# Kernel tuning notes

Measured on AMD Instinct MI355X. Metric: run time of the kernel, lower is better.

## Reference

```python
import jax, jax.numpy as jnp
import numpy as np

WIDTH = 1.0  # radial_width
AMPLITUDE = (WIDTH ** 0.5) * 1.772637204826652  # ~sqrt(pi*width)
BN_EPS = 1e-3  # keras BatchNormalization default


def sine_pos_encoding(seq_len, hidden, dtype):
    # keras_nlp.layers.SinePositionEncoding, max_wavelength=10000
    position = jnp.arange(seq_len, dtype=dtype)
    min_freq = jnp.asarray(1.0 / 10000.0, dtype)
    timescales = min_freq ** (2 * (jnp.arange(hidden) // 2).astype(dtype) / hidden)
    angles = position[:, None] * timescales[None, :]  # [T, H]
    odd = (jnp.arange(hidden) % 2).astype(dtype)
    return jnp.sin(angles) * (1 - odd) + jnp.cos(angles) * odd


def setup_inputs() -> dict:
    key = jax.random.key(0)
    ks = jax.random.split(key, 4)
    B, T, C, F, K, L = 16, 4096, 8, 64, 11, 4096
    x = jax.random.normal(ks[0], (B, T, C), jnp.float32)
    conv_w = jax.random.normal(ks[1], (K, C, F), jnp.float32) * 0.1
    conv_b = jnp.zeros((F,), jnp.float32)
    gamma = jnp.ones((F,), jnp.float32)
    beta = jnp.zeros((F,), jnp.float32)
    mean = jnp.zeros((F,), jnp.float32)
    var = jnp.ones((F,), jnp.float32)
    # HeNormal init for dense
    dense_w = jax.random.normal(ks[2], (F, L), jnp.float32) * (2.0 / F) ** 0.5
    dense_b = jnp.zeros((L,), jnp.float32)
    return dict(x=x, conv_w=conv_w, conv_b=conv_b, gamma=gamma, beta=beta,
                mean=mean, var=var, dense_w=dense_w, dense_b=dense_b)


def reference(x, conv_w, conv_b, gamma, beta, mean, var, dense_w, dense_b):
    B, T, C = x.shape
    F = conv_w.shape[-1]
    L = dense_w.shape[-1]
    # Conv1D same padding -> [B, T, F]
    h = jax.lax.conv_general_dilated(x, conv_w, (1,), 'SAME',
                                     dimension_numbers=('NWC', 'WIO', 'NWC')) + conv_b
    # BatchNorm (inference form)
    h = (h - mean) / jnp.sqrt(var + BN_EPS) * gamma + beta
    # Softmax over time axis
    h = jax.nn.softmax(h, axis=1)
    # sine positional encoding added
    h = h + sine_pos_encoding(T, F, x.dtype)
    # Dense with sigmoid, rescale to [-1, 1]
    d = jax.nn.sigmoid(h @ dense_w + dense_b) * 2.0 - 1.0  # [B, T, L]
    # ReductionLayer: sum over time -> shift weights [B, L]
    shift = jnp.sum(d, axis=1)
    # ShiftingLayer: Gaussian RBF warp matrix then matmul
    idx_in = jnp.arange(1, T + 1, dtype=x.dtype)                       # [T]
    scale = jnp.asarray(T / L, x.dtype)
    idx_sh = (jnp.arange(1, L + 1, dtype=x.dtype) + shift) * scale     # [B, L]
    M = idx_in[None, None, :] - idx_sh[:, :, None]                     # [B, L, T]
    M = jnp.exp(-(M * M) / WIDTH) / AMPLITUDE
    return jnp.matmul(M, x)  # [B, L, C]
```

## Files before the change

### kernel.cpp

```cpp
#include <hip/hip_runtime.h>
#include <stdint.h>

#define BB 16
#define TT 4096
#define CC 8
#define FF 64
#define KW 11
#define LL 4096

#define L2E 1.442695040888963f
#define NCONV (BB * (TT / 64))

typedef __attribute__((ext_vector_type(8))) short short8;
typedef __attribute__((ext_vector_type(16))) float floatx16;

__device__ float e_buf[(size_t)BB * TT * FF];
__device__ float sumpart[NCONV * FF];
__device__ float shift_part[(size_t)BB * 32 * LL];

__device__ __forceinline__ unsigned short f2b(float f) {
    union { float f; uint32_t i; } v; v.f = f;
    uint32_t x = v.i;
    return (unsigned short)((x + 0x7fffu + ((x >> 16) & 1u)) >> 16);
}
__device__ __forceinline__ float b2f(unsigned short u) {
    union { uint32_t i; float f; } v; v.i = ((uint32_t)u) << 16; return v.f;
}

#define DOT8(acc, ra, rb, wp) \
    acc = fmaf(ra.x, (wp)[0], acc); acc = fmaf(ra.y, (wp)[1], acc); \
    acc = fmaf(ra.z, (wp)[2], acc); acc = fmaf(ra.w, (wp)[3], acc); \
    acc = fmaf(rb.x, (wp)[4], acc); acc = fmaf(rb.y, (wp)[5], acc); \
    acc = fmaf(rb.z, (wp)[6], acc); acc = fmaf(rb.w, (wp)[7], acc);

__global__ __launch_bounds__(256) void k_convsplit(
        const float* __restrict__ x, const float* __restrict__ cw,
        const float* __restrict__ cb, const float* __restrict__ gm,
        const float* __restrict__ bt, const float* __restrict__ mn,
        const float* __restrict__ vr, const float* __restrict__ dw,
        unsigned short* __restrict__ Wt) {
    if (blockIdx.x >= NCONV) {
        const int idx  = (blockIdx.x - NCONV) * 256 + threadIdx.x;
        const int j    = idx & 7;
        const int ln   = (idx >> 3) & 31;
        const int half = (idx >> 8) & 1;
        const int kf   = (idx >> 9) & 3;
        const int lt   = idx >> 11;
        const int l = lt * 32 + ln;
        const int k = kf * 16 + half * 8 + j;
        const float v = dw[(size_t)k * LL + l] * (-L2E);
        const unsigned short hi = f2b(v);
        const unsigned short lo = f2b(v - b2f(hi));
        Wt[idx] = hi;
        Wt[262144 + idx] = lo;
        return;
    }
    __shared__ __align__(16) float xsm[(64 + KW - 1) * CC];
    __shared__ float red[4 * FF];
    const int tid = threadIdx.x;
    const int b  = blockIdx.x / (TT / 64);
    const int t0 = (blockIdx.x % (TT / 64)) * 64;
    const int f = tid & 63, ts = tid >> 6;

    float wreg[KW * CC];
#pragma unroll
    for (int kc = 0; kc < KW * CC; ++kc) wreg[kc] = cw[kc * FF + f];

    for (int i = tid; i < (64 + KW - 1) * CC; i += 256) {
        int row = i >> 3, c = i & 7;
        int t = t0 - (KW / 2) + row;
        xsm[i] = (t >= 0 && t < TT) ? x[((size_t)b * TT + t) * CC + c] : 0.0f;
    }
    const float s  = gm[f] * rsqrtf(vr[f] + 1e-3f);
    const float bb = bt[f] + (cb[f] - mn[f]) * s;
    const float s2 = s * L2E, b2 = bb * L2E;
    __syncthreads();

    float* eb = e_buf + ((size_t)b * TT + t0) * FF + f;
    const float4* xv = (const float4*)xsm;
    float esum = 0.f;
#pragma unroll 1
    for (int c = 0; c < 4; ++c) {
        const int tb = c * 16 + ts * 4;
        float a0 = 0.f, a1 = 0.f, a2 = 0.f, a3 = 0.f;
#pragma unroll
        for (int k = 0; k < KW + 3; ++k) {
            const float4 ra = xv[(tb + k) * 2];
            const float4 rb = xv[(tb + k) * 2 + 1];
            if (k <= 10)           { DOT8(a0, ra, rb, wreg + k * 8); }
            if (k >= 1 && k <= 11) { DOT8(a1, ra, rb, wreg + (k - 1) * 8); }
            if (k >= 2 && k <= 12) { DOT8(a2, ra, rb, wreg + (k - 2) * 8); }
            if (k >= 3)            { DOT8(a3, ra, rb, wreg + (k - 3) * 8); }
        }
        float e0 = __builtin_amdgcn_exp2f(fmaf(a0, s2, b2));
        float e1 = __builtin_amdgcn_exp2f(fmaf(a1, s2, b2));
        float e2 = __builtin_amdgcn_exp2f(fmaf(a2, s2, b2));
        float e3 = __builtin_amdgcn_exp2f(fmaf(a3, s2, b2));
        eb[(tb + 0) * FF] = e0;
        eb[(tb + 1) * FF] = e1;
        eb[(tb + 2) * FF] = e2;
        eb[(tb + 3) * FF] = e3;
        esum += (e0 + e1) + (e2 + e3);
    }
    red[ts * FF + f] = esum;
    __syncthreads();
    if (ts == 0)
        sumpart[blockIdx.x * FF + f] = red[f] + red[FF + f] + red[2 * FF + f] + red[3 * FF + f];
}

__global__ __launch_bounds__(512) void k_main(
        const unsigned short* __restrict__ Wt,
        const float* __restrict__ db, float* __restrict__ dummy) {
    __shared__ __align__(16) unsigned short As[16384];

    const int tid = threadIdx.x;
    const int b  = blockIdx.y;
    const int t0 = blockIdx.x * 128;
    const int f = tid & 63, tq = tid >> 6;

    float se = 0.f;
    const float* sp = sumpart + (size_t)b * 64 * FF + f;
#pragma unroll 8
    for (int j = 0; j < 64; ++j) se += sp[j * FF];
    const float inv_se = 1.0f / se;

    const float tsf = exp2f(-0.20762050586796017f * (float)(f & ~1));
    const int kfh = ((f >> 4) << 1) | ((f >> 3) & 1);
    const int jj  = f & 7;
    const float ang0 = (float)(t0 + tq) * tsf;
    const float dA = 8.0f * tsf;
    float sv = sinf(ang0), cv = cosf(ang0);
    const float sd = sinf(dA), cd = cosf(dA);

    const float* eb = e_buf + ((size_t)b * TT + t0) * FF + f;
#pragma unroll 4
    for (int i = 0; i < 16; ++i) {
        const int tt = tq + 8 * i;
        float ev = eb[tt * FF];
        float p = (f & 1) ? cv : sv;
        float h = fmaf(ev, inv_se, p);
        const unsigned short hi = f2b(h);
        const unsigned short lo = f2b(h - b2f(hi));
        const int off = ((tt >> 5) * 8 + kfh) * 256 + (tt & 31) * 8 + jj;
        As[off] = hi;
        As[8192 + off] = lo;
        float ns = fmaf(sv, cd, cv * sd);
        float nc = fmaf(cv, cd, -(sv * sd));
        sv = ns; cv = nc;
    }
    __syncthreads();

    const int lane = tid & 63;
    const int wv   = tid >> 6;
    const int half = lane >> 5;
    const int ln31 = lane & 31;
    const int vbase = (half << 9) | (ln31 << 4);
    const char* Ab = (const char*)As;
    const char* Wb = (const char*)Wt;

#pragma unroll 1
    for (int i = 0; i < 16; ++i) {
        const int lt = (i + 2 * wv) & 15;
        const int ltile = lt * 8 + wv;
        const int lbase = ltile * 32;
        const char* wp = Wb + ((size_t)ltile << 12) + vbase;
        short8 Whi[4], Wlo[4];
#pragma unroll
        for (int kf = 0; kf < 4; ++kf) {
            Whi[kf] = *reinterpret_cast<const short8*>(wp + kf * 1024);
            Wlo[kf] = *reinterpret_cast<const short8*>(wp + 524288 + kf * 1024);
        }
        const float dbn = db[lbase + ln31] * (-L2E);

        float ss[4] = {0.f, 0.f, 0.f, 0.f};
#pragma unroll
        for (int nt = 0; nt < 4; ++nt) {
            floatx16 acc;
#pragma unroll
            for (int r = 0; r < 16; ++r) acc[r] = dbn;
            __builtin_amdgcn_s_setprio(1);
#pragma unroll
            for (int kf = 0; kf < 4; ++kf) {
                const int ao = (nt * 8 + kf * 2) << 9;
                short8 Ahi = *reinterpret_cast<const short8*>(Ab + ao + vbase);
                short8 Alo = *reinterpret_cast<const short8*>(Ab + 16384 + ao + vbase);
                acc = __builtin_amdgcn_mfma_f32_32x32x16_bf16(Ahi, Whi[kf], acc, 0, 0, 0);
                acc = __builtin_amdgcn_mfma_f32_32x32x16_bf16(Alo, Whi[kf], acc, 0, 0, 0);
                acc = __builtin_amdgcn_mfma_f32_32x32x16_bf16(Ahi, Wlo[kf], acc, 0, 0, 0);
            }
            __builtin_amdgcn_s_setprio(0);
#pragma unroll
            for (int q = 0; q < 4; ++q) {
                float e0 = __builtin_amdgcn_exp2f(acc[4 * q + 0]);
                float e1 = __builtin_amdgcn_exp2f(acc[4 * q + 1]);
                float e2 = __builtin_amdgcn_exp2f(acc[4 * q + 2]);
                float e3 = __builtin_amdgcn_exp2f(acc[4 * q + 3]);
                float a0 = 1.f + e0, a1 = 1.f + e1, a2 = 1.f + e2, a3 = 1.f + e3;
                float p01 = a0 * a1, p23 = a2 * a3;
                float num = fmaf(a0 + a1, p23, (a2 + a3) * p01);
                ss[q] = fmaf(num, __builtin_amdgcn_rcpf(p01 * p23), ss[q]);
            }
        }
        float ssum = (ss[0] + ss[1]) + (ss[2] + ss[3]);
        ssum += __shfl_xor(ssum, 32);
        if (half == 0)
            shift_part[((size_t)b * 32 + blockIdx.x) * LL + lbase + ln31] = ssum;
    }
}

__global__ __launch_bounds__(256) void k_warp(
        const float* __restrict__ x, float* __restrict__ out) {
    const int idx = blockIdx.x * 256 + threadIdx.x;
    const int l = idx & (LL - 1);
    const int b = idx >> 12;
    float S = 0.f;
    const float* sp = shift_part + (size_t)b * 32 * LL + l;
#pragma unroll 8
    for (int tt = 0; tt < 32; ++tt) S += sp[tt * LL];
    const float sh = fmaf(2.0f, S, -(float)TT);
    const float scale = (float)TT / (float)LL;
    const float center = ((float)(l + 1) + sh) * scale;
    const float R = 7.0f;
    int tlo = (int)ceilf(center - 1.0f - R);
    int thi = (int)floorf(center - 1.0f + R);
    if (tlo < 0) tlo = 0;
    if (thi > TT - 1) thi = TT - 1;
    float acc[CC];
#pragma unroll
    for (int c = 0; c < CC; ++c) acc[c] = 0.f;
    const float inv_amp = (float)(1.0 / 1.772637204826652);
    for (int t = tlo; t <= thi; ++t) {
        float d = (float)(t + 1) - center;
        float w = __expf(-d * d) * inv_amp;
        const float4 x0 = *reinterpret_cast<const float4*>(x + ((size_t)b * TT + t) * CC);
        const float4 x1 = *reinterpret_cast<const float4*>(x + ((size_t)b * TT + t) * CC + 4);
        acc[0] = fmaf(w, x0.x, acc[0]);
        acc[1] = fmaf(w, x0.y, acc[1]);
        acc[2] = fmaf(w, x0.z, acc[2]);
        acc[3] = fmaf(w, x0.w, acc[3]);
        acc[4] = fmaf(w, x1.x, acc[4]);
        acc[5] = fmaf(w, x1.y, acc[5]);
        acc[6] = fmaf(w, x1.z, acc[6]);
        acc[7] = fmaf(w, x1.w, acc[7]);
    }
    float* o = out + (size_t)idx * CC;
    *reinterpret_cast<float4*>(o)     = make_float4(acc[0], acc[1], acc[2], acc[3]);
    *reinterpret_cast<float4*>(o + 4) = make_float4(acc[4], acc[5], acc[6], acc[7]);
}

extern "C" void kernel_launch(void* const* d_in, const int* in_sizes, int n_in,
                              void* d_out, int out_size, void* d_ws, size_t ws_size,
                              hipStream_t stream) {
    const float* x  = (const float*)d_in[0];
    const float* cw = (const float*)d_in[1];
    const float* cb = (const float*)d_in[2];
    const float* gm = (const float*)d_in[3];
    const float* bt = (const float*)d_in[4];
    const float* mn = (const float*)d_in[5];
    const float* vr = (const float*)d_in[6];
    const float* dw = (const float*)d_in[7];
    const float* db = (const float*)d_in[8];

    unsigned short* Wt = (unsigned short*)d_ws;

    k_convsplit<<<NCONV + (FF * LL) / 256, 256, 0, stream>>>(
        x, cw, cb, gm, bt, mn, vr, dw, Wt);
    k_main<<<dim3(TT / 128, BB), 512, 0, stream>>>(Wt, db, nullptr);
    k_warp<<<(BB * LL) / 256, 256, 0, stream>>>(x, (float*)d_out);
}
```

Baseline: 190.3 us.

## Hoist A fragments into registers and ping-pong MFMA accumulators with sigmoid epilogue

```diff
diff --git a/kernel.cpp b/kernel.cpp
--- a/kernel.cpp
+++ b/kernel.cpp
@@ -108,7 +108,21 @@
         sumpart[blockIdx.x * FF + f] = red[f] + red[FF + f] + red[2 * FF + f] + red[3 * FF + f];
 }
 
-__global__ __launch_bounds__(512) void k_main(
+__device__ __forceinline__ void epi(const floatx16 &acc, float *ss) {
+#pragma unroll
+    for (int q = 0; q < 4; ++q) {
+        float e0 = __builtin_amdgcn_exp2f(acc[4 * q + 0]);
+        float e1 = __builtin_amdgcn_exp2f(acc[4 * q + 1]);
+        float e2 = __builtin_amdgcn_exp2f(acc[4 * q + 2]);
+        float e3 = __builtin_amdgcn_exp2f(acc[4 * q + 3]);
+        float a0 = 1.f + e0, a1 = 1.f + e1, a2 = 1.f + e2, a3 = 1.f + e3;
+        float p01 = a0 * a1, p23 = a2 * a3;
+        float num = fmaf(a0 + a1, p23, (a2 + a3) * p01);
+        ss[q] = fmaf(num, __builtin_amdgcn_rcpf(p01 * p23), ss[q]);
+    }
+}
+
+__global__ __launch_bounds__(512, 1) void k_main(
         const unsigned short* __restrict__ Wt,
         const float* __restrict__ db, float* __restrict__ dummy) {
     __shared__ __align__(16) unsigned short As[16384];
@@ -158,6 +172,28 @@
     const char* Ab = (const char*)As;
     const char* Wb = (const char*)Wt;
 
+    short8 Af[4][4], Al[4][4];
+#pragma unroll
+    for (int nt = 0; nt < 4; ++nt)
+#pragma unroll
+        for (int kf = 0; kf < 4; ++kf) {
+            const int ao = (nt * 8 + kf * 2) << 9;
+            Af[nt][kf] = *reinterpret_cast<const short8*>(Ab + ao + vbase);
+            Al[nt][kf] = *reinterpret_cast<const short8*>(Ab + 16384 + ao + vbase);
+            asm volatile("" : "+v"(Af[nt][kf]), "+v"(Al[nt][kf]));
+        }
+
+#define MFMA3(ACC, NT, KF) \
+    ACC = __builtin_amdgcn_mfma_f32_32x32x16_bf16(Af[NT][KF], Whi[KF], ACC, 0, 0, 0); \
+    ACC = __builtin_amdgcn_mfma_f32_32x32x16_bf16(Al[NT][KF], Whi[KF], ACC, 0, 0, 0); \
+    ACC = __builtin_amdgcn_mfma_f32_32x32x16_bf16(Af[NT][KF], Wlo[KF], ACC, 0, 0, 0);
+
+#define CHAIN(ACC, NT) \
+    { for (int r = 0; r < 16; ++r) ACC[r] = dbn; } \
+    __builtin_amdgcn_s_setprio(1); \
+    MFMA3(ACC, NT, 0) MFMA3(ACC, NT, 1) MFMA3(ACC, NT, 2) MFMA3(ACC, NT, 3) \
+    __builtin_amdgcn_s_setprio(0);
+
 #pragma unroll 1
     for (int i = 0; i < 16; ++i) {
         const int lt = (i + 2 * wv) & 15;
@@ -173,39 +209,23 @@
         const float dbn = db[lbase + ln31] * (-L2E);
 
         float ss[4] = {0.f, 0.f, 0.f, 0.f};
-#pragma unroll
-        for (int nt = 0; nt < 4; ++nt) {
-            floatx16 acc;
-#pragma unroll
-            for (int r = 0; r < 16; ++r) acc[r] = dbn;
-            __builtin_amdgcn_s_setprio(1);
-#pragma unroll
-            for (int kf = 0; kf < 4; ++kf) {
-                const int ao = (nt * 8 + kf * 2) << 9;
-                short8 Ahi = *reinterpret_cast<const short8*>(Ab + ao + vbase);
-                short8 Alo = *reinterpret_cast<const short8*>(Ab + 16384 + ao + vbase);
-                acc = __builtin_amdgcn_mfma_f32_32x32x16_bf16(Ahi, Whi[kf], acc, 0, 0, 0);
-                acc = __builtin_amdgcn_mfma_f32_32x32x16_bf16(Alo, Whi[kf], acc, 0, 0, 0);
-                acc = __builtin_amdgcn_mfma_f32_32x32x16_bf16(Ahi, Wlo[kf], acc, 0, 0, 0);
-            }
-            __builtin_amdgcn_s_setprio(0);
-#pragma unroll
-            for (int q = 0; q < 4; ++q) {
-                float e0 = __builtin_amdgcn_exp2f(acc[4 * q + 0]);
-                float e1 = __builtin_amdgcn_exp2f(acc[4 * q + 1]);
-                float e2 = __builtin_amdgcn_exp2f(acc[4 * q + 2]);
-                float e3 = __builtin_amdgcn_exp2f(acc[4 * q + 3]);
-                float a0 = 1.f + e0, a1 = 1.f + e1, a2 = 1.f + e2, a3 = 1.f + e3;
-                float p01 = a0 * a1, p23 = a2 * a3;
-                float num = fmaf(a0 + a1, p23, (a2 + a3) * p01);
-                ss[q] = fmaf(num, __builtin_amdgcn_rcpf(p01 * p23), ss[q]);
-            }
-        }
+        floatx16 accA, accB;
+        CHAIN(accA, 0)
+        CHAIN(accB, 1)
+        epi(accA, ss);
+        CHAIN(accA, 2)
+        epi(accB, ss);
+        CHAIN(accB, 3)
+        epi(accA, ss);
+        epi(accB, ss);
+
         float ssum = (ss[0] + ss[1]) + (ss[2] + ss[3]);
         ssum += __shfl_xor(ssum, 32);
         if (half == 0)
             shift_part[((size_t)b * 32 + blockIdx.x) * LL + lbase + ln31] = ssum;
     }
+#undef CHAIN
+#undef MFMA3
 }
 
 __global__ __launch_bounds__(256) void k_warp(
```

New measurement: 187.6 us. Within noise of the previous version (-1.4%).
